# Kernel tuning notes

Hardware: AMD Instinct MI355X
Metric: run time of the kernel (lower is better)

## Reference

```python
import jax, jax.numpy as jnp
import numpy as np

U, I, D, E = 50000, 100000, 64, 4000000
N = U + I
N_LAYERS = 3


def setup_inputs() -> dict:
    key = jax.random.key(0)
    k1, k2, k3, k4, k5 = jax.random.split(key, 5)
    user_emb = jax.random.normal(k1, (U, D), dtype=jnp.float32) * 0.1
    item_emb = jax.random.normal(k2, (I, D), dtype=jnp.float32) * 0.1
    edge_rows = jax.random.randint(k3, (E,), 0, N, dtype=jnp.int32)
    edge_cols = jax.random.randint(k4, (E,), 0, N, dtype=jnp.int32)
    # normalized-Laplacian-like positive values
    edge_vals = jax.random.uniform(k5, (E,), dtype=jnp.float32) * 0.01
    return {"user_emb": user_emb, "item_emb": item_emb,
            "edge_rows": edge_rows, "edge_cols": edge_cols,
            "edge_vals": edge_vals}


def _spmm(rows, cols, vals, x):
    # y[r] = sum_{e: rows[e]==r} vals[e] * x[cols[e]]   (COO SpMM)
    gathered = x[cols] * vals[:, None]          # [E, D]
    return jax.ops.segment_sum(gathered, rows, num_segments=N)


def reference(user_emb, item_emb, edge_rows, edge_cols, edge_vals):
    ego = jnp.concatenate([user_emb, item_emb], axis=0)  # [N, D]
    acc = ego
    for _ in range(N_LAYERS):
        ego = _spmm(edge_rows, edge_cols, edge_vals, ego)
        acc = acc + ego
    all_emb = acc / jnp.float32(N_LAYERS + 1)  # mean over stacked layer outputs
    return all_emb[:U], all_emb[U:]
```

## Files before the change

kernel.cpp:

```cpp
#include <hip/hip_runtime.h>
#include <hip/hip_fp16.h>

#define U_CNT 50000
#define I_CNT 100000
#define DIM 64
#define E_CNT 4000000
#define N_CNT (U_CNT + I_CNT)

#define BROWS 512
#define NBUK ((N_CNT + BROWS - 1) / BROWS)
#define CAP  16384
#define CHUNK_A 8192
#define NBLK_A ((E_CNT + CHUNK_A - 1) / CHUNK_A)
#define EPT (CHUNK_A / 512)

typedef unsigned long long u64;
typedef unsigned int u32;
typedef unsigned short u16;
typedef float f32x2 __attribute__((ext_vector_type(2)));
typedef _Float16 f16x2 __attribute__((ext_vector_type(2)));

__device__ __forceinline__ u16 f2h(float f) {
    return __half_as_ushort(__float2half(f));
}
__device__ __forceinline__ float h2f(u16 h) {
    return __half2float(__ushort_as_half(h));
}

__global__ __launch_bounds__(256) void init_kernel(
    const float* __restrict__ user_emb,
    const float* __restrict__ item_emb,
    u16* __restrict__ ego)
{
    long idx = (long)blockIdx.x * blockDim.x + threadIdx.x;
    const long total = (long)N_CNT * DIM / 4;
    if (idx >= total) return;
    long f = idx * 4;
    const long ubound = (long)U_CNT * DIM;
    float4 v;
    if (f < ubound) v = *(const float4*)(user_emb + f);
    else            v = *(const float4*)(item_emb + (f - ubound));
    ushort4 b;
    b.x = f2h(v.x); b.y = f2h(v.y); b.z = f2h(v.z); b.w = f2h(v.w);
    *(ushort4*)(ego + f) = b;
}

__global__ __launch_bounds__(512) void bucket_scatter(
    const int* __restrict__ rows, const int* __restrict__ cols,
    const float* __restrict__ vals, int* __restrict__ bucket_cursor,
    u64* __restrict__ pck1)
{
    __shared__ int hist[NBUK];
    __shared__ int base[NBUK];
    const int tid = threadIdx.x;
    if (tid < NBUK) hist[tid] = 0;
    __syncthreads();

    long e0 = (long)blockIdx.x * CHUNK_A;
    long e1 = e0 + CHUNK_A; if (e1 > E_CNT) e1 = E_CNT;

    u32 saved[EPT];
    int n = 0;
    for (long e = e0 + tid; e < e1; e += 512) {
        int r = rows[e];
        int b = r >> 9;
        int k = atomicAdd(&hist[b], 1);
        saved[n++] = ((u32)b << 22) | ((u32)(r & (BROWS - 1)) << 13) | (u32)k;
    }
    __syncthreads();

    if (tid < NBUK) {
        int h = hist[tid];
        base[tid] = h ? atomicAdd(&bucket_cursor[tid], h) : 0;
    }
    __syncthreads();

    n = 0;
    for (long e = e0 + tid; e < e1; e += 512) {
        u32 s = saved[n++];
        int b  = (int)(s >> 22);
        int rl = (int)((s >> 13) & (BROWS - 1));
        int k  = (int)(s & 8191);
        int pos = base[b] + k;
        if (pos < CAP) {
            u32 vcode = ((u32)f2h(vals[e]) >> 1) & 0x3FFFu;
            u64 packed = ((u64)vcode << 27) | ((u64)(u32)rl << 18) | (u32)cols[e];
            pck1[(long)b * CAP + pos] = packed;
        }
    }
}

__global__ __launch_bounds__(1024) void bucket_scan(
    const int* __restrict__ bucket_cursor, int* __restrict__ bucket_base)
{
    __shared__ int sm[1024];
    int tid = threadIdx.x;
    int c = (tid < NBUK) ? bucket_cursor[tid] : 0;
    int v = (c > CAP) ? CAP : c;
    sm[tid] = v;
    __syncthreads();
    for (int off = 1; off < 1024; off <<= 1) {
        int t = (tid >= off) ? sm[tid - off] : 0;
        __syncthreads();
        sm[tid] += t;
        __syncthreads();
    }
    if (tid < NBUK) bucket_base[tid] = sm[tid] - v;
}

__global__ __launch_bounds__(512) void bucket_sort(
    const u64* __restrict__ pck1,
    const int* __restrict__ bucket_cursor,
    const int* __restrict__ bucket_base,
    u32* __restrict__ pck,
    int* __restrict__ row_start)
{
    __shared__ int h[BROWS];
    __shared__ int sm[BROWS];
    __shared__ int cur[BROWS];
    const int b   = blockIdx.x;
    const int tid = threadIdx.x;
    int cnt = bucket_cursor[b]; if (cnt > CAP) cnt = CAP;
    const int S = bucket_base[b];
    const u64* src = pck1 + (long)b * CAP;

    h[tid] = 0;
    __syncthreads();
    for (int i = tid; i < cnt; i += 512)
        atomicAdd(&h[(int)((src[i] >> 18) & (BROWS - 1))], 1);
    __syncthreads();

    int v = h[tid];
    sm[tid] = v;
    __syncthreads();
    for (int off = 1; off < BROWS; off <<= 1) {
        int t = (tid >= off) ? sm[tid - off] : 0;
        __syncthreads();
        sm[tid] += t;
        __syncthreads();
    }
    int excl = sm[tid] - v;
    cur[tid] = excl;
    int idx = (b << 9) + tid;
    if (idx <= N_CNT) row_start[idx] = S + excl;
    __syncthreads();

    for (int i = tid; i < cnt; i += 512) {
        u64 pv = src[i];
        int rl = (int)((pv >> 18) & (BROWS - 1));
        int p = atomicAdd(&cur[rl], 1);
        pck[S + p] = (u32)(((pv >> 27) << 18) | (pv & 0x3FFFFu));
    }
}

__global__ __launch_bounds__(256) void spmm_csr(
    const int* __restrict__ row_start,
    const u32* __restrict__ pck,
    const u16* __restrict__ x,
    u16* __restrict__ y,
    float* __restrict__ outacc,
    int mode)
{
    const int lane = threadIdx.x & 63;
    const int g    = lane >> 3;
    const int h    = lane & 7;
    int w = (int)(((long)blockIdx.x * blockDim.x + threadIdx.x) >> 6);
    if (w >= N_CNT / 2) return;
    const int r0 = w << 1;
    int s0  = row_start[r0];
    int mid = row_start[r0 + 1];
    int e1  = row_start[r0 + 2];

    f32x2 A0 = {0.f, 0.f}, A1 = {0.f, 0.f}, A2 = {0.f, 0.f}, A3 = {0.f, 0.f};
    f32x2 B0 = {0.f, 0.f}, B1 = {0.f, 0.f}, B2 = {0.f, 0.f}, B3 = {0.f, 0.f};

#define EDGE_BODY(P, Q0, Q1, Q2, Q3)                                        \
    {                                                                       \
        u32 c  = (P) & 0x3FFFFu;                                            \
        u32 hv = ((P) >> 17) & 0x7FFEu;                                     \
        u32 vv = hv | (hv << 16);                                           \
        f16x2 vh = __builtin_bit_cast(f16x2, vv);                           \
        const uint4 xb = *(const uint4*)(x + ((long)c << 6) + (h << 3));    \
        Q0 += __builtin_bit_cast(f16x2, xb.x) * vh;                         \
        Q1 += __builtin_bit_cast(f16x2, xb.y) * vh;                         \
        Q2 += __builtin_bit_cast(f16x2, xb.z) * vh;                         \
        Q3 += __builtin_bit_cast(f16x2, xb.w) * vh;                         \
    }

#define DO_ITERS(N, PK, Q0, Q1, Q2, Q3)                                     \
    {                                                                       \
        _Pragma("unroll")                                                   \
        for (int j = 0; j < (N); ++j) {                                     \
            u32 p = (u32)__shfl((int)(PK), (j << 3) + g);                   \
            EDGE_BODY(p, Q0, Q1, Q2, Q3)                                    \
        }                                                                   \
    }

#define ROW_CHUNK(REM, PK, Q0, Q1, Q2, Q3)                                  \
    {                                                                       \
        int it = ((REM) >= 64) ? 8 : (((REM) + 7) >> 3);                    \
        switch (it) {                                                       \
            case 8: DO_ITERS(8, PK, Q0, Q1, Q2, Q3) break;                  \
            case 7: DO_ITERS(7, PK, Q0, Q1, Q2, Q3) break;                  \
            case 6: DO_ITERS(6, PK, Q0, Q1, Q2, Q3) break;                  \
            case 5: DO_ITERS(5, PK, Q0, Q1, Q2, Q3) break;                  \
            case 4: DO_ITERS(4, PK, Q0, Q1, Q2, Q3) break;                  \
            case 3: DO_ITERS(3, PK, Q0, Q1, Q2, Q3) break;                  \
            case 2: DO_ITERS(2, PK, Q0, Q1, Q2, Q3) break;                  \
            default: DO_ITERS(1, PK, Q0, Q1, Q2, Q3) break;                 \
        }                                                                   \
    }

    int base0 = s0, base1 = mid;
    while (base0 < mid || base1 < e1) {
        int rem0 = mid - base0;
        int rem1 = e1 - base1;
        u32 pk0 = 0u, pk1 = 0u;
        if (base0 + lane < mid) pk0 = __builtin_nontemporal_load(pck + base0 + lane);
        if (base1 + lane < e1)  pk1 = __builtin_nontemporal_load(pck + base1 + lane);
        f16x2 Hz = {(_Float16)0, (_Float16)0};
        f16x2 H0 = Hz, H1 = Hz, H2 = Hz, H3 = Hz;
        f16x2 K0 = Hz, K1 = Hz, K2 = Hz, K3 = Hz;
        if (rem0 > 0) ROW_CHUNK(rem0, pk0, H0, H1, H2, H3)
        if (rem1 > 0) ROW_CHUNK(rem1, pk1, K0, K1, K2, K3)
        #pragma unroll
        for (int off = 8; off < 64; off <<= 1) {
            H0 += __builtin_bit_cast(f16x2, (u32)__shfl_xor((int)__builtin_bit_cast(u32, H0), off));
            H1 += __builtin_bit_cast(f16x2, (u32)__shfl_xor((int)__builtin_bit_cast(u32, H1), off));
            H2 += __builtin_bit_cast(f16x2, (u32)__shfl_xor((int)__builtin_bit_cast(u32, H2), off));
            H3 += __builtin_bit_cast(f16x2, (u32)__shfl_xor((int)__builtin_bit_cast(u32, H3), off));
            K0 += __builtin_bit_cast(f16x2, (u32)__shfl_xor((int)__builtin_bit_cast(u32, K0), off));
            K1 += __builtin_bit_cast(f16x2, (u32)__shfl_xor((int)__builtin_bit_cast(u32, K1), off));
            K2 += __builtin_bit_cast(f16x2, (u32)__shfl_xor((int)__builtin_bit_cast(u32, K2), off));
            K3 += __builtin_bit_cast(f16x2, (u32)__shfl_xor((int)__builtin_bit_cast(u32, K3), off));
        }
        A0.x += (float)H0.x; A0.y += (float)H0.y;
        A1.x += (float)H1.x; A1.y += (float)H1.y;
        A2.x += (float)H2.x; A2.y += (float)H2.y;
        A3.x += (float)H3.x; A3.y += (float)H3.y;
        B0.x += (float)K0.x; B0.y += (float)K0.y;
        B1.x += (float)K1.x; B1.y += (float)K1.y;
        B2.x += (float)K2.x; B2.y += (float)K2.y;
        B3.x += (float)K3.x; B3.y += (float)K3.y;
        base0 += 64; base1 += 64;
    }
#undef ROW_CHUNK
#undef DO_ITERS
#undef EDGE_BODY

    float a0 = g ? B0.x : A0.x, a1 = g ? B0.y : A0.y;
    float a2 = g ? B1.x : A1.x, a3 = g ? B1.y : A1.y;
    float a4 = g ? B2.x : A2.x, a5 = g ? B2.y : A2.y;
    float a6 = g ? B3.x : A3.x, a7 = g ? B3.y : A3.y;

    if (g < 2) {
        long o = ((long)(r0 + g) << 6) + (h << 3);
        if (mode < 2) {
            ushort4 y0, y1;
            y0.x = f2h(a0); y0.y = f2h(a1); y0.z = f2h(a2); y0.w = f2h(a3);
            y1.x = f2h(a4); y1.y = f2h(a5); y1.z = f2h(a6); y1.w = f2h(a7);
            *(ushort4*)(y + o)     = y0;
            *(ushort4*)(y + o + 4) = y1;
        }
        if (mode != 1) {
            const ushort4 xl = *(const ushort4*)(x + o);
            const ushort4 xh = *(const ushort4*)(x + o + 4);
            float o0 = h2f(xl.x), o1 = h2f(xl.y), o2 = h2f(xl.z), o3 = h2f(xl.w);
            float o4 = h2f(xh.x), o5 = h2f(xh.y), o6 = h2f(xh.z), o7 = h2f(xh.w);
            float4 t0, t1;
            if (mode == 0) {
                t0.x = o0 + a0; t0.y = o1 + a1; t0.z = o2 + a2; t0.w = o3 + a3;
                t1.x = o4 + a4; t1.y = o5 + a5; t1.z = o6 + a6; t1.w = o7 + a7;
            } else {
                t0 = *(const float4*)(outacc + o);
                t1 = *(const float4*)(outacc + o + 4);
                t0.x = (t0.x + o0 + a0) * 0.25f; t0.y = (t0.y + o1 + a1) * 0.25f;
                t0.z = (t0.z + o2 + a2) * 0.25f; t0.w = (t0.w + o3 + a3) * 0.25f;
                t1.x = (t1.x + o4 + a4) * 0.25f; t1.y = (t1.y + o5 + a5) * 0.25f;
                t1.z = (t1.z + o6 + a6) * 0.25f; t1.w = (t1.w + o7 + a7) * 0.25f;
            }
            *(float4*)(outacc + o)     = t0;
            *(float4*)(outacc + o + 4) = t1;
        }
    }
}

extern "C" void kernel_launch(void* const* d_in, const int* in_sizes, int n_in,
                              void* d_out, int out_size, void* d_ws, size_t ws_size,
                              hipStream_t stream) {
    const float* user_emb = (const float*)d_in[0];
    const float* item_emb = (const float*)d_in[1];
    const int*   rows     = (const int*)d_in[2];
    const int*   cols     = (const int*)d_in[3];
    const float* vals     = (const float*)d_in[4];
    float* outacc = (float*)d_out;

    char* ws = (char*)d_ws;
    u32*  pck  = (u32*)ws;                        ws += (size_t)E_CNT * 4;
    u64*  pck1 = (u64*)ws;
    u16*  ego  = (u16*)ws;
    u16*  nxt  = ego + (size_t)N_CNT * DIM;
    {
        size_t a = (size_t)NBUK * CAP * 8;
        size_t b = (size_t)N_CNT * DIM * 2 * 2;
        ws += (a > b) ? a : b;
    }
    int* row_start     = (int*)ws;                ws += (size_t)(N_CNT + 16) * 4;
    int* bucket_cursor = (int*)ws;                ws += 1024 * 4;
    int* bucket_base   = (int*)ws;                ws += 1024 * 4;

    hipMemsetAsync(bucket_cursor, 0, (size_t)NBUK * 4, stream);

    bucket_scatter<<<NBLK_A, 512, 0, stream>>>(rows, cols, vals, bucket_cursor, pck1);
    bucket_scan<<<1, 1024, 0, stream>>>(bucket_cursor, bucket_base);
    bucket_sort<<<NBUK, 512, 0, stream>>>(pck1, bucket_cursor, bucket_base, pck, row_start);

    const long total_f4 = (long)N_CNT * DIM / 4;
    const int  vgrid = (int)((total_f4 + 255) / 256);
    init_kernel<<<vgrid, 256, 0, stream>>>(user_emb, item_emb, ego);

    const int spmm_grid = ((N_CNT / 2) * 64 + 255) / 256;
    spmm_csr<<<spmm_grid, 256, 0, stream>>>(row_start, pck, ego, nxt, outacc, 0);
    spmm_csr<<<spmm_grid, 256, 0, stream>>>(row_start, pck, nxt, ego, outacc, 1);
    spmm_csr<<<spmm_grid, 256, 0, stream>>>(row_start, pck, ego, nxt, outacc, 2);
}
```

Baseline: 318.5 us.

## Restructure SpMM row loop to issue eight independent gathers per step

The per-row edge loop is rewritten. One packed-edge load per lane now covers 32 edges of each of the two rows, and all eight row gathers are issued up front before the FMAs. This replaces the variable-length switch over the shuffle-plus-gather sequence. The cross-lane reduction and the fp32 conversion move out of the loop, so each row accumulates entirely in fp16 instead of in fp32 per 64-edge chunk. The aim is more memory-level parallelism and less per-iteration overhead. The costs are wasted gathers on padded lanes (zero weight, index 0) and more fp16 rounding on high-degree rows.

```diff
diff --git a/kernel.cpp b/kernel.cpp
--- a/kernel.cpp
+++ b/kernel.cpp
@@ -17,7 +17,6 @@
 typedef unsigned long long u64;
 typedef unsigned int u32;
 typedef unsigned short u16;
-typedef float f32x2 __attribute__((ext_vector_type(2)));
 typedef _Float16 f16x2 __attribute__((ext_vector_type(2)));
 
 __device__ __forceinline__ u16 f2h(float f) {
@@ -171,87 +170,78 @@
     int mid = row_start[r0 + 1];
     int e1  = row_start[r0 + 2];
 
-    f32x2 A0 = {0.f, 0.f}, A1 = {0.f, 0.f}, A2 = {0.f, 0.f}, A3 = {0.f, 0.f};
-    f32x2 B0 = {0.f, 0.f}, B1 = {0.f, 0.f}, B2 = {0.f, 0.f}, B3 = {0.f, 0.f};
-
-#define EDGE_BODY(P, Q0, Q1, Q2, Q3)                                        \
-    {                                                                       \
-        u32 c  = (P) & 0x3FFFFu;                                            \
-        u32 hv = ((P) >> 17) & 0x7FFEu;                                     \
-        u32 vv = hv | (hv << 16);                                           \
-        f16x2 vh = __builtin_bit_cast(f16x2, vv);                           \
-        const uint4 xb = *(const uint4*)(x + ((long)c << 6) + (h << 3));    \
-        Q0 += __builtin_bit_cast(f16x2, xb.x) * vh;                         \
-        Q1 += __builtin_bit_cast(f16x2, xb.y) * vh;                         \
-        Q2 += __builtin_bit_cast(f16x2, xb.z) * vh;                         \
-        Q3 += __builtin_bit_cast(f16x2, xb.w) * vh;                         \
-    }
-
-#define DO_ITERS(N, PK, Q0, Q1, Q2, Q3)                                     \
-    {                                                                       \
-        _Pragma("unroll")                                                   \
-        for (int j = 0; j < (N); ++j) {                                     \
-            u32 p = (u32)__shfl((int)(PK), (j << 3) + g);                   \
-            EDGE_BODY(p, Q0, Q1, Q2, Q3)                                    \
-        }                                                                   \
-    }
-
-#define ROW_CHUNK(REM, PK, Q0, Q1, Q2, Q3)                                  \
-    {                                                                       \
-        int it = ((REM) >= 64) ? 8 : (((REM) + 7) >> 3);                    \
-        switch (it) {                                                       \
-            case 8: DO_ITERS(8, PK, Q0, Q1, Q2, Q3) break;                  \
-            case 7: DO_ITERS(7, PK, Q0, Q1, Q2, Q3) break;                  \
-            case 6: DO_ITERS(6, PK, Q0, Q1, Q2, Q3) break;                  \
-            case 5: DO_ITERS(5, PK, Q0, Q1, Q2, Q3) break;                  \
-            case 4: DO_ITERS(4, PK, Q0, Q1, Q2, Q3) break;                  \
-            case 3: DO_ITERS(3, PK, Q0, Q1, Q2, Q3) break;                  \
-            case 2: DO_ITERS(2, PK, Q0, Q1, Q2, Q3) break;                  \
-            default: DO_ITERS(1, PK, Q0, Q1, Q2, Q3) break;                 \
-        }                                                                   \
-    }
-
+    const f16x2 Hz = {(_Float16)0, (_Float16)0};
+    f16x2 H0 = Hz, H1 = Hz, H2 = Hz, H3 = Hz;
+    f16x2 K0 = Hz, K1 = Hz, K2 = Hz, K3 = Hz;
+
+    const int ll = lane & 31;
     int base0 = s0, base1 = mid;
+
+#define GATHER(P) (*(const uint4*)(x + ((long)((P) & 0x3FFFFu) << 6) + (h << 3)))
+#define VH(P) __builtin_bit_cast(f16x2, (u32)((((P) >> 17) & 0x7FFEu) * 0x10001u))
+#define FMA4(XB, VHV, Q0, Q1, Q2, Q3)                                       \
+        Q0 += __builtin_bit_cast(f16x2, (XB).x) * (VHV);                     \
+        Q1 += __builtin_bit_cast(f16x2, (XB).y) * (VHV);                     \
+        Q2 += __builtin_bit_cast(f16x2, (XB).z) * (VHV);                     \
+        Q3 += __builtin_bit_cast(f16x2, (XB).w) * (VHV);
+
     while (base0 < mid || base1 < e1) {
-        int rem0 = mid - base0;
-        int rem1 = e1 - base1;
-        u32 pk0 = 0u, pk1 = 0u;
-        if (base0 + lane < mid) pk0 = __builtin_nontemporal_load(pck + base0 + lane);
-        if (base1 + lane < e1)  pk1 = __builtin_nontemporal_load(pck + base1 + lane);
-        f16x2 Hz = {(_Float16)0, (_Float16)0};
-        f16x2 H0 = Hz, H1 = Hz, H2 = Hz, H3 = Hz;
-        f16x2 K0 = Hz, K1 = Hz, K2 = Hz, K3 = Hz;
-        if (rem0 > 0) ROW_CHUNK(rem0, pk0, H0, H1, H2, H3)
-        if (rem1 > 0) ROW_CHUNK(rem1, pk1, K0, K1, K2, K3)
-        #pragma unroll
-        for (int off = 8; off < 64; off <<= 1) {
-            H0 += __builtin_bit_cast(f16x2, (u32)__shfl_xor((int)__builtin_bit_cast(u32, H0), off));
-            H1 += __builtin_bit_cast(f16x2, (u32)__shfl_xor((int)__builtin_bit_cast(u32, H1), off));
-            H2 += __builtin_bit_cast(f16x2, (u32)__shfl_xor((int)__builtin_bit_cast(u32, H2), off));
-            H3 += __builtin_bit_cast(f16x2, (u32)__shfl_xor((int)__builtin_bit_cast(u32, H3), off));
-            K0 += __builtin_bit_cast(f16x2, (u32)__shfl_xor((int)__builtin_bit_cast(u32, K0), off));
-            K1 += __builtin_bit_cast(f16x2, (u32)__shfl_xor((int)__builtin_bit_cast(u32, K1), off));
-            K2 += __builtin_bit_cast(f16x2, (u32)__shfl_xor((int)__builtin_bit_cast(u32, K2), off));
-            K3 += __builtin_bit_cast(f16x2, (u32)__shfl_xor((int)__builtin_bit_cast(u32, K3), off));
-        }
-        A0.x += (float)H0.x; A0.y += (float)H0.y;
-        A1.x += (float)H1.x; A1.y += (float)H1.y;
-        A2.x += (float)H2.x; A2.y += (float)H2.y;
-        A3.x += (float)H3.x; A3.y += (float)H3.y;
-        B0.x += (float)K0.x; B0.y += (float)K0.y;
-        B1.x += (float)K1.x; B1.y += (float)K1.y;
-        B2.x += (float)K2.x; B2.y += (float)K2.y;
-        B3.x += (float)K3.x; B3.y += (float)K3.y;
-        base0 += 64; base1 += 64;
-    }
-#undef ROW_CHUNK
-#undef DO_ITERS
-#undef EDGE_BODY
-
-    float a0 = g ? B0.x : A0.x, a1 = g ? B0.y : A0.y;
-    float a2 = g ? B1.x : A1.x, a3 = g ? B1.y : A1.y;
-    float a4 = g ? B2.x : A2.x, a5 = g ? B2.y : A2.y;
-    float a6 = g ? B3.x : A3.x, a7 = g ? B3.y : A3.y;
+        int  idx = (lane < 32) ? (base0 + ll) : (base1 + ll);
+        int  lim = (lane < 32) ? mid : e1;
+        u32 pk = 0u;
+        if (idx < lim) pk = __builtin_nontemporal_load(pck + idx);
+
+        u32 p00 = (u32)__shfl((int)pk,      g);
+        u32 p01 = (u32)__shfl((int)pk,  8 + g);
+        u32 p02 = (u32)__shfl((int)pk, 16 + g);
+        u32 p03 = (u32)__shfl((int)pk, 24 + g);
+        u32 p10 = (u32)__shfl((int)pk, 32 + g);
+        u32 p11 = (u32)__shfl((int)pk, 40 + g);
+        u32 p12 = (u32)__shfl((int)pk, 48 + g);
+        u32 p13 = (u32)__shfl((int)pk, 56 + g);
+
+        const uint4 xa0 = GATHER(p00);
+        const uint4 xa1 = GATHER(p01);
+        const uint4 xa2 = GATHER(p02);
+        const uint4 xa3 = GATHER(p03);
+        const uint4 xb0 = GATHER(p10);
+        const uint4 xb1 = GATHER(p11);
+        const uint4 xb2 = GATHER(p12);
+        const uint4 xb3 = GATHER(p13);
+
+        FMA4(xa0, VH(p00), H0, H1, H2, H3)
+        FMA4(xa1, VH(p01), H0, H1, H2, H3)
+        FMA4(xa2, VH(p02), H0, H1, H2, H3)
+        FMA4(xa3, VH(p03), H0, H1, H2, H3)
+        FMA4(xb0, VH(p10), K0, K1, K2, K3)
+        FMA4(xb1, VH(p11), K0, K1, K2, K3)
+        FMA4(xb2, VH(p12), K0, K1, K2, K3)
+        FMA4(xb3, VH(p13), K0, K1, K2, K3)
+
+        base0 += 32; base1 += 32;
+        if (base0 > mid) base0 = mid;
+        if (base1 > e1)  base1 = e1;
+    }
+#undef FMA4
+#undef VH
+#undef GATHER
+
+    #pragma unroll
+    for (int off = 8; off < 64; off <<= 1) {
+        H0 += __builtin_bit_cast(f16x2, (u32)__shfl_xor((int)__builtin_bit_cast(u32, H0), off));
+        H1 += __builtin_bit_cast(f16x2, (u32)__shfl_xor((int)__builtin_bit_cast(u32, H1), off));
+        H2 += __builtin_bit_cast(f16x2, (u32)__shfl_xor((int)__builtin_bit_cast(u32, H2), off));
+        H3 += __builtin_bit_cast(f16x2, (u32)__shfl_xor((int)__builtin_bit_cast(u32, H3), off));
+        K0 += __builtin_bit_cast(f16x2, (u32)__shfl_xor((int)__builtin_bit_cast(u32, K0), off));
+        K1 += __builtin_bit_cast(f16x2, (u32)__shfl_xor((int)__builtin_bit_cast(u32, K1), off));
+        K2 += __builtin_bit_cast(f16x2, (u32)__shfl_xor((int)__builtin_bit_cast(u32, K2), off));
+        K3 += __builtin_bit_cast(f16x2, (u32)__shfl_xor((int)__builtin_bit_cast(u32, K3), off));
+    }
+
+    float a0 = g ? (float)K0.x : (float)H0.x, a1 = g ? (float)K0.y : (float)H0.y;
+    float a2 = g ? (float)K1.x : (float)H1.x, a3 = g ? (float)K1.y : (float)H1.y;
+    float a4 = g ? (float)K2.x : (float)H2.x, a5 = g ? (float)K2.y : (float)H2.y;
+    float a6 = g ? (float)K3.x : (float)H3.x, a7 = g ? (float)K3.y : (float)H3.y;
 
     if (g < 2) {
         long o = ((long)(r0 + g) << 6) + (h << 3);
```

Measured after the change: 316.8 us. Within noise of the previous version (-0.5%).
